# Kernel optimization log

Measured on AMD Instinct MI355X. Metric: run time of the kernel, lower is better.

The kernel has to match this reference:

```python
import jax, jax.numpy as jnp
import numpy as np
from jax import lax

B, IN, HID, OUT = 32, 1024, 1024, 1024
NN, NS, NH = 1000, 64, 4          # n_paths/num_neurons, num_states, attn heads
NSTEPS = NS * 10                   # 640 SDE steps
GROUPS = 10                        # python loop groups in original BICEPLayer
T_HORIZON = 1.0


def setup_inputs() -> dict:
    key = jax.random.key(0)
    ks = jax.random.split(key, 16)
    def n(k, shape, s=0.02):
        return jax.random.normal(k, shape, jnp.float32) * s
    z = lambda *s: jnp.zeros(s, jnp.float32)
    return {
        "x": jax.random.normal(ks[0], (B, IN), jnp.float32),
        "noise": jax.random.normal(ks[1], (B, NN, NSTEPS), jnp.float32),
        "W_emb": n(ks[2], (NN * NS, IN)), "b_emb": z(NN * NS),
        "w_ih": n(ks[3], (4 * NS, NS), 0.1), "w_hh": n(ks[4], (4 * NS, NS), 0.1),
        "b_ih": z(4 * NS), "b_hh": z(4 * NS),
        "w_in": n(ks[5], (3 * NS, NS), 0.1), "b_in": z(3 * NS),
        "w_out": n(ks[6], (NS, NS), 0.1), "b_out": z(NS),
        "W_fix": jax.random.normal(ks[7], (HID, NS), jnp.float32),  # torch.randn dim-fix linear
        "W_inproj": n(ks[8], (NN, IN)), "b_inproj": z(NN),
        "conv_w": n(ks[9], (1, NSTEPS + 1, 3), 0.05), "conv_b": z(1),
        "W_bout": n(ks[10], (HID, NN)), "b_bout": z(HID),
        "decay_rate": jnp.float32(0.1),
        "W_fuse": n(ks[11], (HID, 2 * HID)), "b_fuse": z(HID),
        "W_proj": n(ks[12], (OUT, HID)), "b_proj": z(OUT),
    }


def _forward(x, noise, W_emb, b_emb, w_ih, w_hh, b_ih, b_hh, w_in, b_in,
             w_out, b_out, W_fix, W_inproj, b_inproj, conv_w, conv_b,
             W_bout, b_bout, decay_rate, W_fuse, b_fuse, W_proj, b_proj):
    Bsz = x.shape[0]
    # ---- ENN branch ----
    ns = (x @ W_emb.T + b_emb).reshape(Bsz, NN, NS)

    def lstm_step(carry, xt):  # xt [B, NS]
        h, c = carry
        g = xt @ w_ih.T + b_ih + h @ w_hh.T + b_hh
        i, f, gg, o = jnp.split(g, 4, axis=-1)  # torch gate order i,f,g,o
        c = jax.nn.sigmoid(f) * c + jax.nn.sigmoid(i) * jnp.tanh(gg)
        h = jax.nn.sigmoid(o) * jnp.tanh(c)
        return (h, c), h

    h0 = jnp.zeros((Bsz, NS), x.dtype)
    _, hs = lax.scan(lstm_step, (h0, h0), jnp.swapaxes(ns, 0, 1))
    lstm_out = jnp.swapaxes(hs, 0, 1)  # [B, NN, NS]

    qkv = lstm_out @ w_in.T + b_in
    q, k, v = jnp.split(qkv, 3, axis=-1)
    dh = NS // NH
    heads = lambda t: t.reshape(Bsz, NN, NH, dh).transpose(0, 2, 1, 3)
    q, k, v = heads(q), heads(k), heads(v)
    scores = jnp.einsum('bhqd,bhkd->bhqk', q, k) * (1.0 / float(np.sqrt(dh)))
    attn = jax.nn.softmax(scores, axis=-1)
    ctx = jnp.einsum('bhqk,bhkd->bhqd', attn, v).transpose(0, 2, 1, 3).reshape(Bsz, NN, NS)
    attended = ctx @ w_out.T + b_out
    attn_w = attn.mean(axis=1)  # torch MHA averages heads by default

    enn = jax.nn.relu(attended.mean(axis=1))  # [B, NS]
    enn = enn @ W_fix.T                        # [B, HID] (random dim-fix linear, no bias)

    # ---- BICEP branch (vectorized Brownian SDE over all batches/paths) ----
    fb = jax.nn.sigmoid(x @ W_inproj.T + b_inproj)  # [B, NN]
    # original uses .item() -> detached scalars, only first 10 feedback values
    f_full = jnp.repeat(lax.stop_gradient(fb[:, :GROUPS]), NN // GROUPS, axis=1)  # [B, NN]
    dt = T_HORIZON / NSTEPS
    sq = float(np.sqrt(dt))
    dr = lax.stop_gradient(decay_rate)  # .item() in original

    def sde_step(Xc, nt):  # Euler-Maruyama: dX = -decay*X dt + feedback dW
        Xn = Xc * (1.0 - dr * dt) + f_full * sq * nt
        return Xn, Xn

    _, Xs = lax.scan(sde_step, jnp.zeros((Bsz, NN), x.dtype), jnp.moveaxis(noise, 2, 0))
    paths = jnp.concatenate([jnp.zeros((1, Bsz, NN), x.dtype), Xs], axis=0)  # [T+1, B, NN]
    paths = jnp.moveaxis(paths, 0, 1)  # [B, NSTEPS+1, NN] -> channels = time

    agg = lax.conv_general_dilated(paths, conv_w, (1,), ((1, 1),),
                                   dimension_numbers=('NCH', 'OIH', 'NCH'))
    agg = agg[:, 0, :] + conv_b  # [B, NN]
    bicep = agg @ W_bout.T + b_bout  # [B, HID]

    # ---- fusion (dropout is identity in eval) ----
    fused = jnp.concatenate([enn, bicep], axis=-1) @ W_fuse.T + b_fuse
    output = fused @ W_proj.T + b_proj
    return output, enn, bicep, attn_w


def reference(x, noise, W_emb, b_emb, w_ih, w_hh, b_ih, b_hh, w_in, b_in,
              w_out, b_out, W_fix, W_inproj, b_inproj, conv_w, conv_b,
              W_bout, b_bout, decay_rate, W_fuse, b_fuse, W_proj, b_proj):
    return _forward(x, noise, W_emb, b_emb, w_ih, w_hh, b_ih, b_hh, w_in, b_in,
                    w_out, b_out, W_fix, W_inproj, b_inproj, conv_w, conv_b,
                    W_bout, b_bout, decay_rate, W_fuse, b_fuse, W_proj, b_proj)
```

## Files before the change

kernel.cpp:

```cpp
#include <hip/hip_runtime.h>
#include <hip/hip_bf16.h>
#include <math.h>

#define BATCH 32

typedef short bf16x8 __attribute__((ext_vector_type(8)));
typedef float f32x4 __attribute__((ext_vector_type(4)));

__device__ __forceinline__ float sigmoidf_(float x){ return 1.0f/(1.0f + __expf(-x)); }
__device__ __forceinline__ unsigned short f2bf(float x){
  unsigned u = __float_as_uint(x);
  unsigned r = (u + 0x7FFFu + ((u>>16)&1u)) >> 16;
  return (unsigned short)r;
}
__device__ __forceinline__ float sig2(float x){
  return __builtin_amdgcn_rcpf(1.0f + __builtin_amdgcn_exp2f(x * -1.44269504f));
}
__device__ __forceinline__ float tanh2(float x){
  return 1.0f - 2.0f*__builtin_amdgcn_rcpf(1.0f + __builtin_amdgcn_exp2f(x * 2.88539008f));
}
__device__ __forceinline__ f32x4 unpk4(uint2 p){
  f32x4 r;
  r[0] = __uint_as_float(p.x << 16);
  r[1] = __uint_as_float(p.x & 0xffff0000u);
  r[2] = __uint_as_float(p.y << 16);
  r[3] = __uint_as_float(p.y & 0xffff0000u);
  return r;
}

__global__ __launch_bounds__(256) void k12_emb_pre(const float* __restrict__ x,
    const float* __restrict__ W_emb, const float* __restrict__ b_emb,
    const float* __restrict__ W_inp, const float* __restrict__ b_inp,
    const float* __restrict__ w_ih, const float* __restrict__ b_ih, const float* __restrict__ b_hh,
    float* __restrict__ fb, unsigned short* __restrict__ preh)
{
  __shared__ __align__(16) float xl[BATCH][256];
  __shared__ float red[64][33];
  __shared__ __align__(16) float nsl2[32][68];
  const int tid = threadIdx.x;
  const int jt = tid >> 4;
  const int seg = tid & 15;
  const int blk = blockIdx.x;
  const bool isemb = (blk < 1000);
  const float* wr_[4];
  #pragma unroll
  for (int jj=0;jj<4;jj++){
    if (isemb) wr_[jj] = W_emb + (size_t)(blk*64 + jt*4 + jj) * 1024;
    else { int t2 = (blk-1000)*64 + jt*4 + jj; if (t2 > 999) t2 = 999; wr_[jj] = W_inp + (size_t)t2 * 1024; }
  }
  float acc[4][32];
  #pragma unroll
  for (int jj=0;jj<4;jj++)
    #pragma unroll
    for (int b=0;b<32;b++) acc[jj][b]=0.f;
  for (int c=0;c<4;c++){
    __syncthreads();
    for (int f = tid; f < 2048; f += 256){
      int b = f >> 6; int col = (f & 63) << 2;
      *(float4*)&xl[b][col] = *(const float4*)&x[b*1024 + c*256 + col];
    }
    __syncthreads();
    #pragma unroll
    for (int ii=0; ii<4; ii++){
      float4 wv[4];
      #pragma unroll
      for (int jj=0;jj<4;jj++) wv[jj] = *(const float4*)&wr_[jj][c*256 + ii*64 + seg*4];
      #pragma unroll
      for (int b=0;b<32;b++){
        float4 xv = *(const float4*)&xl[b][ii*64 + seg*4];
        #pragma unroll
        for (int jj=0;jj<4;jj++){
          acc[jj][b] = fmaf(wv[jj].x, xv.x, acc[jj][b]);
          acc[jj][b] = fmaf(wv[jj].y, xv.y, acc[jj][b]);
          acc[jj][b] = fmaf(wv[jj].z, xv.z, acc[jj][b]);
          acc[jj][b] = fmaf(wv[jj].w, xv.w, acc[jj][b]);
        }
      }
    }
  }
  #pragma unroll
  for (int jj=0;jj<4;jj++){
    #pragma unroll
    for (int b=0;b<32;b++){
      float v = acc[jj][b];
      v += __shfl_xor(v, 1);
      v += __shfl_xor(v, 2);
      v += __shfl_xor(v, 4);
      v += __shfl_xor(v, 8);
      if (seg == 0) red[jt*4+jj][b] = v;
    }
  }
  __syncthreads();
  #pragma unroll
  for (int it=0; it<8; it++){
    int idx = it*256 + tid;
    int b = idx >> 6, jl = idx & 63;
    float v = red[jl][b];
    if (isemb){
      nsl2[b][jl] = v + b_emb[blk*64 + jl];
    } else {
      int jin = (blk-1000)*64 + jl;
      if (jin < 1000) fb[b*1000 + jin] = sigmoidf_(v + b_inp[jin]);
    }
  }
  if (!isemb) return;
  __syncthreads();
  const int j = tid;
  const int pcol = (j & 63)*4 + (j >> 6);
  float wreg[64];
  const float* wr = w_ih + j*64;
  #pragma unroll
  for (int k=0;k<64;k+=4){
    float4 v = *(const float4*)&wr[k];
    wreg[k]=v.x; wreg[k+1]=v.y; wreg[k+2]=v.z; wreg[k+3]=v.w;
  }
  float bias = b_ih[j] + b_hh[j];
  for (int b=0;b<32;b++){
    float a0=0,a1=0,a2=0,a3=0;
    #pragma unroll
    for (int k=0;k<64;k+=4){
      float4 nv = *(const float4*)&nsl2[b][k];
      a0=fmaf(nv.x,wreg[k],a0);   a1=fmaf(nv.y,wreg[k+1],a1);
      a2=fmaf(nv.z,wreg[k+2],a2); a3=fmaf(nv.w,wreg[k+3],a3);
    }
    preh[(size_t)(b*1000+blk)*256 + pcol] = f2bf((a0+a1)+(a2+a3) + bias);
  }
}

__global__ __launch_bounds__(256) void k3_lstm_sde(
  const unsigned short* __restrict__ preh, unsigned short* __restrict__ lstmT,
  const float* __restrict__ w_hh,
  const float* __restrict__ noise, const float* __restrict__ fb,
  const float* __restrict__ conv_w, const float* __restrict__ decay_p,
  float* __restrict__ S0, float* __restrict__ S1, float* __restrict__ S2)
{
  __shared__ __align__(16) unsigned char shraw[8192];
  const int tid = threadIdx.x;
  if (blockIdx.x < 8){
    unsigned short* hls = (unsigned short*)shraw;
    const int b0 = blockIdx.x * 4;
    const int w = tid >> 6;
    const int lane = tid & 63;
    const int nl = lane & 15;
    const int g  = lane >> 4;
    const int r  = nl & 3;
    for (int i = tid; i < 640; i += 256) hls[i] = 0;
    bf16x8 A[4][2];
    #pragma unroll
    for (int tt=0; tt<4; tt++){
      const int rt = 4*w + tt;
      const float* wsrc = w_hh + (size_t)((nl&3)*64 + 4*rt + (nl>>2))*64;
      #pragma unroll
      for (int kh=0; kh<2; kh++){
        bf16x8 f;
        #pragma unroll
        for (int i=0;i<8;i++) f[i] = (short)f2bf(wsrc[kh*32 + 8*g + i]);
        A[tt][kh] = f;
      }
    }
    const int jg = 16*w + 4*(nl>>2) + g;
    const int bat = b0 + r;
    const unsigned short* pp = preh + (size_t)bat*256000 + jg*4;
    uint2 P[4];
    #pragma unroll
    for (int s=0;s<4;s++) P[s] = *(const uint2*)(pp + (size_t)s*256);
    const int rdA = r*80 + (g ^ r)*8;
    const int wr = r*80 + ((jg>>3) ^ r)*8 + (jg & 7);
    unsigned short* lt = lstmT + ((size_t)bat*64 + jg)*1000;
    const bool s1 = (nl & 4) != 0, s2 = (nl & 8) != 0;
    float c = 0.f;
    unsigned ph[4];
    __syncthreads();
    int buf = 0;
    for (int tb=0; tb<1000; tb+=8){
      #pragma unroll
      for (int u=0;u<8;u++){
        bf16x8 B0 = *(const bf16x8*)&hls[buf*320 + rdA];
        bf16x8 B1 = *(const bf16x8*)&hls[buf*320 + rdA + 32];
        const int slot = u & 3;
        f32x4 Cp = unpk4(P[slot]);
        int tp = tb + u + 4; if (tp > 999) tp = 999;
        P[slot] = *(const uint2*)(pp + (size_t)tp*256);
        f32x4 D0 = __builtin_amdgcn_mfma_f32_16x16x32_bf16(A[0][0], B0, Cp, 0,0,0);
        D0 = __builtin_amdgcn_mfma_f32_16x16x32_bf16(A[0][1], B1, D0, 0,0,0);
        f32x4 D1 = __builtin_amdgcn_mfma_f32_16x16x32_bf16(A[1][0], B0, Cp, 0,0,0);
        D1 = __builtin_amdgcn_mfma_f32_16x16x32_bf16(A[1][1], B1, D1, 0,0,0);
        f32x4 D2 = __builtin_amdgcn_mfma_f32_16x16x32_bf16(A[2][0], B0, Cp, 0,0,0);
        D2 = __builtin_amdgcn_mfma_f32_16x16x32_bf16(A[2][1], B1, D2, 0,0,0);
        f32x4 D3 = __builtin_amdgcn_mfma_f32_16x16x32_bf16(A[3][0], B0, Cp, 0,0,0);
        D3 = __builtin_amdgcn_mfma_f32_16x16x32_bf16(A[3][1], B1, D3, 0,0,0);
        float g0 = s2 ? (s1 ? D3[0] : D2[0]) : (s1 ? D1[0] : D0[0]);
        float g1 = s2 ? (s1 ? D3[1] : D2[1]) : (s1 ? D1[1] : D0[1]);
        float g2 = s2 ? (s1 ? D3[2] : D2[2]) : (s1 ? D1[2] : D0[2]);
        float g3 = s2 ? (s1 ? D3[3] : D2[3]) : (s1 ? D1[3] : D0[3]);
        float iv = sig2(g0), fv = sig2(g1), gv = tanh2(g2), ov = sig2(g3);
        c = fv*c + iv*gv;
        float h = ov * tanh2(c);
        unsigned hb = f2bf(h);
        if (u & 1) ph[u>>1] |= hb << 16; else ph[u>>1] = hb;
        hls[(buf^1)*320 + wr] = (unsigned short)hb;
        asm volatile("s_waitcnt lgkmcnt(0)" ::: "memory");
        __builtin_amdgcn_s_barrier();
        asm volatile("" ::: "memory");
        buf ^= 1;
      }
      *(uint4*)(lt + tb) = make_uint4(ph[0], ph[1], ph[2], ph[3]);
    }
  } else {
    float* cw = (float*)shraw;
    for (int f = tid; f < 641*3; f += 256) cw[f] = conv_w[f];
    __syncthreads();
    int idx = (blockIdx.x - 8)*256 + tid;
    if (idx < 32000){
      int b = idx / 1000, n = idx - b*1000;
      float fcoef = fb[b*1000 + (n/100)];
      float dr = decay_p[0];
      const float dt = 1.0f/640.0f;
      float adec = 1.0f - dr*dt;
      float g = fcoef * sqrtf(dt);
      const float* nptr = noise + (size_t)idx * 640;
      float X=0.f, s0=0.f, s1=0.f, s2=0.f;
      for (int t0=0;t0<640;t0+=4){
        float4 nz = *(const float4*)&nptr[t0];
        float nv[4] = {nz.x, nz.y, nz.z, nz.w};
        #pragma unroll
        for (int u=0;u<4;u++){
          X = fmaf(adec, X, g*nv[u]);
          int t = t0 + u + 1;
          s0 = fmaf(cw[t*3+0], X, s0);
          s1 = fmaf(cw[t*3+1], X, s1);
          s2 = fmaf(cw[t*3+2], X, s2);
        }
      }
      S0[idx]=s0; S1[idx]=s1; S2[idx]=s2;
    }
  }
}

__global__ __launch_bounds__(256) void k4_qkv(const unsigned short* __restrict__ lstmT,
  const float* __restrict__ w_in, const float* __restrict__ b_in,
  unsigned short* __restrict__ Qb, unsigned short* __restrict__ Kb, unsigned short* __restrict__ Vt)
{
  __shared__ __align__(16) float wl[192*64];
  __shared__ float bl[192];
  const int tid = threadIdx.x;
  for (int i=tid;i<3072;i+=256) ((float4*)wl)[i] = ((const float4*)w_in)[i];
  if (tid < 192) bl[tid] = b_in[tid];
  __syncthreads();
  const int rl = tid & 127, dh = tid >> 7;
  const int rn = blockIdx.x*128 + rl;
  const int b = rn >> 10, n = rn & 1023;
  const bool valid = (n < 1000);
  const int nc = valid ? n : 999;
  float row[64];
  #pragma unroll
  for (int k=0;k<64;k++){
    unsigned v = lstmT[((size_t)b*64 + k)*1000 + nc];
    row[k] = valid ? __uint_as_float(v << 16) : 0.f;
  }
  for (int dc=0; dc<12; dc++){
    const int d0 = dh*96 + dc*8;
    float acc[8];
    #pragma unroll
    for (int u=0;u<8;u++) acc[u] = bl[d0+u];
    #pragma unroll
    for (int k=0;k<64;k+=4){
      float4 rv = *(const float4*)&row[k];
      #pragma unroll
      for (int u=0;u<8;u++){
        float4 wv = *(const float4*)&wl[(d0+u)*64 + k];
        acc[u]=fmaf(rv.x,wv.x,acc[u]); acc[u]=fmaf(rv.y,wv.y,acc[u]);
        acc[u]=fmaf(rv.z,wv.z,acc[u]); acc[u]=fmaf(rv.w,wv.w,acc[u]);
      }
    }
    unsigned short pk[8];
    #pragma unroll
    for (int u=0;u<8;u++) pk[u] = valid ? f2bf(acc[u]) : (unsigned short)0;
    if (d0 + 8 <= 64){
      *(bf16x8*)&Qb[(size_t)rn*64 + d0] = *(bf16x8*)pk;
    } else if (d0 + 8 <= 128){
      *(bf16x8*)&Kb[(size_t)rn*64 + (d0-64)] = *(bf16x8*)pk;
    } else {
      int dv = d0 - 128;
      #pragma unroll
      for (int u=0;u<8;u++) Vt[((size_t)b*64 + dv+u)*1024 + n] = pk[u];
    }
  }
}

__global__ __launch_bounds__(256) void k5_attn(
  const unsigned short* __restrict__ Qb, const unsigned short* __restrict__ Kb,
  const unsigned short* __restrict__ Vt,
  float* __restrict__ attn_w, float* __restrict__ ctx)
{
  const int b = blockIdx.x;
  const int qblk = blockIdx.y;
  const int wid = threadIdx.x >> 6;
  const int lane = threadIdx.x & 63;
  const int r = lane & 15, gq = lane >> 4;
  const int q = qblk*64 + wid*16 + r;
  const bool gok = (gq < 2);
  const float SC2 = 0.25f * 1.44269504f;
  const f32x4 z4 = {0.f,0.f,0.f,0.f};

  bf16x8 qf[4];
  #pragma unroll
  for (int h=0; h<4; h++){
    bf16x8 f = {};
    if (gok) f = *(const bf16x8*)&Qb[(((size_t)b*1024)+q)*64 + h*16 + 8*gq];
    qf[h] = f;
  }
  float snv[4];
  #pragma unroll
  for (int h=0; h<4; h++){
    float es = 0.f;
    for (int kk=0; kk<63; kk++){
      bf16x8 kf = {};
      if (gok) kf = *(const bf16x8*)&Kb[(((size_t)b*1024)+(kk*16+r))*64 + h*16 + 8*gq];
      f32x4 d = __builtin_amdgcn_mfma_f32_16x16x32_bf16(kf, qf[h], z4, 0,0,0);
      float e0=__builtin_amdgcn_exp2f(d[0]*SC2), e1=__builtin_amdgcn_exp2f(d[1]*SC2);
      float e2=__builtin_amdgcn_exp2f(d[2]*SC2), e3=__builtin_amdgcn_exp2f(d[3]*SC2);
      if (kk == 62 && !gok){ e0=0;e1=0;e2=0;e3=0; }
      es += (e0+e1)+(e2+e3);
    }
    es += __shfl_xor(es, 16);
    es += __shfl_xor(es, 32);
    snv[h] = 0.25f / es;
  }
  f32x4 cacc[4] = {};
  float* awrow = attn_w + (size_t)b*1000000;
  for (int kkp=0; kkp<31; kkp++){
    const int kk = kkp*2;
    f32x4 aacc0 = z4, aacc1 = z4;
    #pragma unroll
    for (int h=0; h<4; h++){
      bf16x8 kf0 = {}, kf1 = {};
      if (gok){
        kf0 = *(const bf16x8*)&Kb[(((size_t)b*1024)+(kk*16+r))*64 + h*16 + 8*gq];
        kf1 = *(const bf16x8*)&Kb[(((size_t)b*1024)+(kk*16+16+r))*64 + h*16 + 8*gq];
      }
      f32x4 d0 = __builtin_amdgcn_mfma_f32_16x16x32_bf16(kf0, qf[h], z4, 0,0,0);
      f32x4 d1 = __builtin_amdgcn_mfma_f32_16x16x32_bf16(kf1, qf[h], z4, 0,0,0);
      float p00=__builtin_amdgcn_exp2f(d0[0]*SC2)*snv[h], p01=__builtin_amdgcn_exp2f(d0[1]*SC2)*snv[h];
      float p02=__builtin_amdgcn_exp2f(d0[2]*SC2)*snv[h], p03=__builtin_amdgcn_exp2f(d0[3]*SC2)*snv[h];
      float p10=__builtin_amdgcn_exp2f(d1[0]*SC2)*snv[h], p11=__builtin_amdgcn_exp2f(d1[1]*SC2)*snv[h];
      float p12=__builtin_amdgcn_exp2f(d1[2]*SC2)*snv[h], p13=__builtin_amdgcn_exp2f(d1[3]*SC2)*snv[h];
      aacc0[0]+=p00; aacc0[1]+=p01; aacc0[2]+=p02; aacc0[3]+=p03;
      aacc1[0]+=p10; aacc1[1]+=p11; aacc1[2]+=p12; aacc1[3]+=p13;
      const int slo = (r + 32*gq) & 63;
      const int shi = (slo + 16) & 63;
      {
        unsigned pa = (unsigned)f2bf(p00) | ((unsigned)f2bf(p01) << 16);
        unsigned pb = (unsigned)f2bf(p02) | ((unsigned)f2bf(p03) << 16);
        int b0_ = __shfl((int)pa, slo), b1_ = __shfl((int)pb, slo);
        int b2_ = __shfl((int)pa, shi), b3_ = __shfl((int)pb, shi);
        union { int i[4]; bf16x8 v; } pu;
        pu.i[0]=b0_; pu.i[1]=b1_; pu.i[2]=b2_; pu.i[3]=b3_;
        bf16x8 pfrag = pu.v;
        if (!gok) pfrag = (bf16x8){};
        bf16x8 vf = {};
        if (gok) vf = *(const bf16x8*)&Vt[(((size_t)b*64) + h*16 + r)*1024 + kk*16 + 8*gq];
        cacc[h] = __builtin_amdgcn_mfma_f32_16x16x32_bf16(vf, pfrag, cacc[h], 0,0,0);
      }
      {
        unsigned pa = (unsigned)f2bf(p10) | ((unsigned)f2bf(p11) << 16);
        unsigned pb = (unsigned)f2bf(p12) | ((unsigned)f2bf(p13) << 16);
        int b0_ = __shfl((int)pa, slo), b1_ = __shfl((int)pb, slo);
        int b2_ = __shfl((int)pa, shi), b3_ = __shfl((int)pb, shi);
        union { int i[4]; bf16x8 v; } pu;
        pu.i[0]=b0_; pu.i[1]=b1_; pu.i[2]=b2_; pu.i[3]=b3_;
        bf16x8 pfrag = pu.v;
        if (!gok) pfrag = (bf16x8){};
        bf16x8 vf = {};
        if (gok) vf = *(const bf16x8*)&Vt[(((size_t)b*64) + h*16 + r)*1024 + kk*16 + 16 + 8*gq];
        cacc[h] = __builtin_amdgcn_mfma_f32_16x16x32_bf16(vf, pfrag, cacc[h], 0,0,0);
      }
    }
    if (q < 1000){
      *(f32x4*)&awrow[(size_t)q*1000 + kk*16 + 4*gq] = aacc0;
      *(f32x4*)&awrow[(size_t)q*1000 + kk*16 + 16 + 4*gq] = aacc1;
    }
  }
  {
    const int kk = 62;
    f32x4 aacc = z4;
    #pragma unroll
    for (int h=0; h<4; h++){
      bf16x8 kf = {};
      if (gok) kf = *(const bf16x8*)&Kb[(((size_t)b*1024)+(kk*16+r))*64 + h*16 + 8*gq];
      f32x4 d = __builtin_amdgcn_mfma_f32_16x16x32_bf16(kf, qf[h], z4, 0,0,0);
      float p0=__builtin_amdgcn_exp2f(d[0]*SC2)*snv[h], p1=__builtin_amdgcn_exp2f(d[1]*SC2)*snv[h];
      float p2=__builtin_amdgcn_exp2f(d[2]*SC2)*snv[h], p3=__builtin_amdgcn_exp2f(d[3]*SC2)*snv[h];
      if (!gok){ p0=0;p1=0;p2=0;p3=0; }
      aacc[0]+=p0; aacc[1]+=p1; aacc[2]+=p2; aacc[3]+=p3;
      unsigned pa = (unsigned)f2bf(p0) | ((unsigned)f2bf(p1) << 16);
      unsigned pb = (unsigned)f2bf(p2) | ((unsigned)f2bf(p3) << 16);
      int slo = (r + 32*gq) & 63;
      int shi = (slo + 16) & 63;
      int b0_ = __shfl((int)pa, slo), b1_ = __shfl((int)pb, slo);
      int b2_ = __shfl((int)pa, shi), b3_ = __shfl((int)pb, shi);
      union { int i[4]; bf16x8 v; } pu;
      pu.i[0]=b0_; pu.i[1]=b1_; pu.i[2]=b2_; pu.i[3]=b3_;
      bf16x8 pfrag = pu.v;
      if (!gok) pfrag = (bf16x8){};
      bf16x8 vf = {};
      if (gok) vf = *(const bf16x8*)&Vt[(((size_t)b*64) + h*16 + r)*1024 + kk*16 + 8*gq];
      cacc[h] = __builtin_amdgcn_mfma_f32_16x16x32_bf16(vf, pfrag, cacc[h], 0,0,0);
    }
    if (q < 1000 && gok){
      *(f32x4*)&awrow[(size_t)q*1000 + kk*16 + 4*gq] = aacc;
    }
  }
  if (q < 1000){
    #pragma unroll
    for (int h=0; h<4; h++){
      f32x4 cv = cacc[h];
      cv[0]*=4.f; cv[1]*=4.f; cv[2]*=4.f; cv[3]*=4.f;
      *(f32x4*)&ctx[(((size_t)b*1024)+q)*64 + h*16 + 4*gq] = cv;
    }
  }
}

__global__ __launch_bounds__(256) void k67_psum_agg(const float* __restrict__ ctx,
  float* __restrict__ psum,
  const float* __restrict__ S0, const float* __restrict__ S1,
  const float* __restrict__ S2, const float* __restrict__ conv_b, float* __restrict__ agg)
{
  if (blockIdx.x < 256){
    __shared__ float part[256];
    const int blk = blockIdx.x;
    const int b = blk >> 3, seg = blk & 7;
    const int t = threadIdx.x, d = t & 63, sg = t >> 6;
    float s = 0.f;
    const int nend = seg*125 + 125;
    for (int n = seg*125 + sg; n < nend; n += 4)
      s += ctx[(((size_t)b*1024)+n)*64 + d];
    part[t] = s;
    __syncthreads();
    if (t < 64) psum[((size_t)b*8 + seg)*64 + t] = part[t] + part[64+t] + part[128+t] + part[192+t];
  } else {
    int i = (blockIdx.x - 256)*256 + threadIdx.x;
    if (i >= 32000) return;
    int n = i % 1000;
    float v = S1[i] + conv_b[0];
    if (n > 0)   v += S0[i-1];
    if (n < 999) v += S2[i+1];
    agg[i] = v;
  }
}

__global__ __launch_bounds__(256) void k68_enn_bicep(const float* __restrict__ psum,
  const float* __restrict__ w_out, const float* __restrict__ b_out,
  const float* __restrict__ W_fix, float* __restrict__ enn_out,
  const float* __restrict__ agg, const float* __restrict__ W_bout,
  const float* __restrict__ b_bout, float* __restrict__ bicep)
{
  if (blockIdx.x < 32){
    __shared__ __align__(16) float csum[64];
    __shared__ __align__(16) float epre[64];
    int b = blockIdx.x, t = threadIdx.x;
    if (t < 64){
      float a = 0;
      #pragma unroll
      for (int s2=0;s2<8;s2++) a += psum[((size_t)b*8 + s2)*64 + t];
      csum[t] = a;
    }
    __syncthreads();
    if (t < 64){
      const float* wr = w_out + t*64;
      float a = 0;
      #pragma unroll
      for (int k=0;k<64;k++) a = fmaf(csum[k], wr[k], a);
      epre[t] = fmaxf(a*(1.0f/1000.0f) + b_out[t], 0.0f);
    }
    __syncthreads();
    for (int m = t; m < 1024; m += 256){
      const float* fr = W_fix + m*64;
      float a = 0;
      #pragma unroll
      for (int k=0;k<64;k+=4){
        float4 e4 = *(const float4*)&epre[k];
        float4 f4 = *(const float4*)&fr[k];
        a=fmaf(e4.x,f4.x,a); a=fmaf(e4.y,f4.y,a); a=fmaf(e4.z,f4.z,a); a=fmaf(e4.w,f4.w,a);
      }
      enn_out[b*1024 + m] = a;
    }
  } else {
    int gt = (blockIdx.x - 32)*256 + threadIdx.x;
    int bb = gt & 31, m = gt >> 5;
    const float* wr = W_bout + (size_t)m*1000;
    const float* ar = agg + bb*1000;
    float a = 0;
    for (int n=0;n<1000;n+=4){
      float4 w4 = *(const float4*)&wr[n];
      float4 a4 = *(const float4*)&ar[n];
      a=fmaf(w4.x,a4.x,a); a=fmaf(w4.y,a4.y,a); a=fmaf(w4.z,a4.z,a); a=fmaf(w4.w,a4.w,a);
    }
    bicep[bb*1024 + m] = a + b_bout[m];
  }
}

__global__ __launch_bounds__(256) void k9_fuse(const float* __restrict__ enn, const float* __restrict__ bic,
  const float* __restrict__ W_fuse, const float* __restrict__ b_fuse, float* __restrict__ fused)
{
  int gt = blockIdx.x*256 + threadIdx.x;
  int bb = gt & 31, m = gt >> 5;
  const float* er = enn + bb*1024;
  const float* br = bic + bb*1024;
  const float* wr = W_fuse + (size_t)m*2048;
  float a = 0;
  for (int jj=0;jj<1024;jj+=4){
    float4 e4 = *(const float4*)&er[jj];
    float4 w4 = *(const float4*)&wr[jj];
    a=fmaf(e4.x,w4.x,a); a=fmaf(e4.y,w4.y,a); a=fmaf(e4.z,w4.z,a); a=fmaf(e4.w,w4.w,a);
  }
  for (int jj=0;jj<1024;jj+=4){
    float4 b4 = *(const float4*)&br[jj];
    float4 w4 = *(const float4*)&wr[1024+jj];
    a=fmaf(b4.x,w4.x,a); a=fmaf(b4.y,w4.y,a); a=fmaf(b4.z,w4.z,a); a=fmaf(b4.w,w4.w,a);
  }
  fused[bb*1024 + m] = a + b_fuse[m];
}

__global__ __launch_bounds__(256) void k10_proj(const float* __restrict__ fused,
  const float* __restrict__ W_proj, const float* __restrict__ b_proj, float* __restrict__ outp)
{
  int gt = blockIdx.x*256 + threadIdx.x;
  int bb = gt & 31, m = gt >> 5;
  const float* fr = fused + bb*1024;
  const float* wr = W_proj + (size_t)m*1024;
  float a = 0;
  for (int jj=0;jj<1024;jj+=4){
    float4 f4 = *(const float4*)&fr[jj];
    float4 w4 = *(const float4*)&wr[jj];
    a=fmaf(f4.x,w4.x,a); a=fmaf(f4.y,w4.y,a); a=fmaf(f4.z,w4.z,a); a=fmaf(f4.w,w4.w,a);
  }
  outp[bb*1024 + m] = a + b_proj[m];
}

extern "C" void kernel_launch(void* const* d_in, const int* in_sizes, int n_in,
                              void* d_out, int out_size, void* d_ws, size_t ws_size,
                              hipStream_t stream)
{
  const float* x       = (const float*)d_in[0];
  const float* noise   = (const float*)d_in[1];
  const float* W_emb   = (const float*)d_in[2];
  const float* b_emb   = (const float*)d_in[3];
  const float* w_ih    = (const float*)d_in[4];
  const float* w_hh    = (const float*)d_in[5];
  const float* b_ih    = (const float*)d_in[6];
  const float* b_hh    = (const float*)d_in[7];
  const float* w_in    = (const float*)d_in[8];
  const float* b_in    = (const float*)d_in[9];
  const float* w_out   = (const float*)d_in[10];
  const float* b_out   = (const float*)d_in[11];
  const float* W_fix   = (const float*)d_in[12];
  const float* W_inp   = (const float*)d_in[13];
  const float* b_inp   = (const float*)d_in[14];
  const float* conv_w  = (const float*)d_in[15];
  const float* conv_b  = (const float*)d_in[16];
  const float* W_bout  = (const float*)d_in[17];
  const float* b_bout  = (const float*)d_in[18];
  const float* decay   = (const float*)d_in[19];
  const float* W_fuse  = (const float*)d_in[20];
  const float* b_fuse  = (const float*)d_in[21];
  const float* W_proj  = (const float*)d_in[22];
  const float* b_proj  = (const float*)d_in[23];

  float* out       = (float*)d_out;
  float* enn_out   = out + 32768;
  float* bicep_out = out + 65536;
  float* attn_out  = out + 98304;

  float* ws    = (float*)d_ws;
  float* fb    = ws;
  unsigned short* preh  = (unsigned short*)(ws + 2080000);
  float* psum  = ws + 6200000;
  unsigned short* lstmT = (unsigned short*)(ws + 10272000);
  float* ctx   = ws + 12320000;
  float* S0    = ws + 14417152;
  float* S1    = ws + 14449152;
  float* S2    = ws + 14481152;
  float* agg   = ws + 14513152;
  float* fused = ws + 14545152;
  unsigned short* Qb = (unsigned short*)(ws + 14577920);
  unsigned short* Kb = Qb + 2097152;
  unsigned short* Vt = Kb + 2097152;

  k12_emb_pre<<<1016, 256, 0, stream>>>(x, W_emb, b_emb, W_inp, b_inp,
                                        w_ih, b_ih, b_hh, fb, preh);
  k3_lstm_sde<<<133, 256, 0, stream>>>(preh, lstmT, w_hh, noise, fb, conv_w, decay, S0, S1, S2);
  k4_qkv<<<256, 256, 0, stream>>>(lstmT, w_in, b_in, Qb, Kb, Vt);
  k5_attn<<<dim3(32,16), 256, 0, stream>>>(Qb, Kb, Vt, attn_out, ctx);
  k67_psum_agg<<<382, 256, 0, stream>>>(ctx, psum, S0, S1, S2, conv_b, agg);
  k68_enn_bicep<<<160, 256, 0, stream>>>(psum, w_out, b_out, W_fix, enn_out,
                                         agg, W_bout, b_bout, bicep_out);
  k9_fuse<<<128, 256, 0, stream>>>(enn_out, bicep_out, W_fuse, b_fuse, fused);
  k10_proj<<<128, 256, 0, stream>>>(fused, W_proj, b_proj, out);
}
```

Before: 985.9 us.

## Use bf16 MFMA for embedding GEMM and split w_ih projection into separate kernel

The fused embedding plus input-projection kernel is split in two. The first kernel computes the large x@W_emb and x@W_inproj GEMMs with bf16 MFMA 16x16x32 instructions, converting fp32 weights and inputs to bf16 on the fly, instead of scalar fp32 FMAs with LDS staging. The second kernel computes the LSTM input-gate pre-activations from the stored ns buffer. This is meant to remove the FMA-bound inner loop, at the cost of an extra launch, a round trip of ns through global memory, and reduced GEMM precision.

```diff
diff --git a/kernel.cpp b/kernel.cpp
--- a/kernel.cpp
+++ b/kernel.cpp
@@ -27,85 +27,82 @@
   r[3] = __uint_as_float(p.y & 0xffff0000u);
   return r;
 }
-
-__global__ __launch_bounds__(256) void k12_emb_pre(const float* __restrict__ x,
+__device__ __forceinline__ bf16x8 pack8(float4 a, float4 b){
+  bf16x8 f;
+  f[0]=(short)f2bf(a.x); f[1]=(short)f2bf(a.y); f[2]=(short)f2bf(a.z); f[3]=(short)f2bf(a.w);
+  f[4]=(short)f2bf(b.x); f[5]=(short)f2bf(b.y); f[6]=(short)f2bf(b.z); f[7]=(short)f2bf(b.w);
+  return f;
+}
+
+__global__ __launch_bounds__(256) void k1_emb(const float* __restrict__ x,
     const float* __restrict__ W_emb, const float* __restrict__ b_emb,
     const float* __restrict__ W_inp, const float* __restrict__ b_inp,
-    const float* __restrict__ w_ih, const float* __restrict__ b_ih, const float* __restrict__ b_hh,
-    float* __restrict__ fb, unsigned short* __restrict__ preh)
-{
-  __shared__ __align__(16) float xl[BATCH][256];
-  __shared__ float red[64][33];
-  __shared__ __align__(16) float nsl2[32][68];
+    float* __restrict__ ns, float* __restrict__ fb)
+{
   const int tid = threadIdx.x;
-  const int jt = tid >> 4;
-  const int seg = tid & 15;
+  const int w = tid >> 6, lane = tid & 63;
+  const int nl = lane & 15, g = lane >> 4;
   const int blk = blockIdx.x;
   const bool isemb = (blk < 1000);
-  const float* wr_[4];
+  const int j0 = (isemb ? blk : (blk - 1000))*64 + w*16;
+  const int arow = j0 + nl;
+  const float* wrow;
+  if (isemb) wrow = W_emb + (size_t)arow*1024;
+  else       wrow = W_inp + (size_t)(arow > 999 ? 999 : arow)*1024;
+  f32x4 D0, D1;
   #pragma unroll
-  for (int jj=0;jj<4;jj++){
-    if (isemb) wr_[jj] = W_emb + (size_t)(blk*64 + jt*4 + jj) * 1024;
-    else { int t2 = (blk-1000)*64 + jt*4 + jj; if (t2 > 999) t2 = 999; wr_[jj] = W_inp + (size_t)t2 * 1024; }
-  }
-  float acc[4][32];
-  #pragma unroll
-  for (int jj=0;jj<4;jj++)
-    #pragma unroll
-    for (int b=0;b<32;b++) acc[jj][b]=0.f;
-  for (int c=0;c<4;c++){
-    __syncthreads();
-    for (int f = tid; f < 2048; f += 256){
-      int b = f >> 6; int col = (f & 63) << 2;
-      *(float4*)&xl[b][col] = *(const float4*)&x[b*1024 + c*256 + col];
-    }
-    __syncthreads();
-    #pragma unroll
-    for (int ii=0; ii<4; ii++){
-      float4 wv[4];
-      #pragma unroll
-      for (int jj=0;jj<4;jj++) wv[jj] = *(const float4*)&wr_[jj][c*256 + ii*64 + seg*4];
-      #pragma unroll
-      for (int b=0;b<32;b++){
-        float4 xv = *(const float4*)&xl[b][ii*64 + seg*4];
-        #pragma unroll
-        for (int jj=0;jj<4;jj++){
-          acc[jj][b] = fmaf(wv[jj].x, xv.x, acc[jj][b]);
-          acc[jj][b] = fmaf(wv[jj].y, xv.y, acc[jj][b]);
-          acc[jj][b] = fmaf(wv[jj].z, xv.z, acc[jj][b]);
-          acc[jj][b] = fmaf(wv[jj].w, xv.w, acc[jj][b]);
-        }
-      }
-    }
-  }
-  #pragma unroll
-  for (int jj=0;jj<4;jj++){
-    #pragma unroll
-    for (int b=0;b<32;b++){
-      float v = acc[jj][b];
-      v += __shfl_xor(v, 1);
-      v += __shfl_xor(v, 2);
-      v += __shfl_xor(v, 4);
-      v += __shfl_xor(v, 8);
-      if (seg == 0) red[jt*4+jj][b] = v;
-    }
-  }
-  __syncthreads();
-  #pragma unroll
-  for (int it=0; it<8; it++){
-    int idx = it*256 + tid;
-    int b = idx >> 6, jl = idx & 63;
-    float v = red[jl][b];
-    if (isemb){
-      nsl2[b][jl] = v + b_emb[blk*64 + jl];
-    } else {
-      int jin = (blk-1000)*64 + jl;
-      if (jin < 1000) fb[b*1000 + jin] = sigmoidf_(v + b_inp[jin]);
-    }
-  }
-  if (!isemb) return;
-  __syncthreads();
+  for (int q=0;q<4;q++){
+    int jr = j0 + 4*g + q;
+    float bb = isemb ? b_emb[jr] : b_inp[jr > 999 ? 999 : jr];
+    D0[q] = bb; D1[q] = bb;
+  }
+  const float* xr0 = x + nl*1024;
+  const float* xr1 = x + (nl+16)*1024;
+  for (int kc=0; kc<8; kc++){
+    float4 wa[4][2];
+    #pragma unroll
+    for (int s=0;s<4;s++){
+      const float* p = wrow + kc*128 + s*32 + 8*g;
+      wa[s][0] = *(const float4*)p;
+      wa[s][1] = *(const float4*)(p+4);
+    }
+    #pragma unroll
+    for (int s=0;s<4;s++){
+      const int k0 = kc*128 + s*32 + 8*g;
+      float4 x00 = *(const float4*)(xr0 + k0);
+      float4 x01 = *(const float4*)(xr0 + k0 + 4);
+      float4 x10 = *(const float4*)(xr1 + k0);
+      float4 x11 = *(const float4*)(xr1 + k0 + 4);
+      bf16x8 A  = pack8(wa[s][0], wa[s][1]);
+      bf16x8 B0 = pack8(x00, x01);
+      bf16x8 B1 = pack8(x10, x11);
+      D0 = __builtin_amdgcn_mfma_f32_16x16x32_bf16(A, B0, D0, 0,0,0);
+      D1 = __builtin_amdgcn_mfma_f32_16x16x32_bf16(A, B1, D1, 0,0,0);
+    }
+  }
+  if (isemb){
+    *(f32x4*)&ns[(size_t)nl*64000 + j0 + 4*g] = D0;
+    *(f32x4*)&ns[(size_t)(nl+16)*64000 + j0 + 4*g] = D1;
+  } else {
+    #pragma unroll
+    for (int q=0;q<4;q++){
+      int jr = j0 + 4*g + q;
+      if (jr < 1000){
+        fb[nl*1000 + jr]      = sig2(D0[q]);
+        fb[(nl+16)*1000 + jr] = sig2(D1[q]);
+      }
+    }
+  }
+}
+
+__global__ __launch_bounds__(256) void k2_pre(const float* __restrict__ ns,
+   const float* __restrict__ w_ih, const float* __restrict__ b_ih, const float* __restrict__ b_hh,
+   unsigned short* __restrict__ preh)
+{
+  __shared__ __align__(16) float nsl[64*64];
+  const int tid = threadIdx.x;
   const int j = tid;
+  const int rn0 = blockIdx.x * 64;
   const int pcol = (j & 63)*4 + (j >> 6);
   float wreg[64];
   const float* wr = w_ih + j*64;
@@ -115,15 +112,18 @@
     wreg[k]=v.x; wreg[k+1]=v.y; wreg[k+2]=v.z; wreg[k+3]=v.w;
   }
   float bias = b_ih[j] + b_hh[j];
-  for (int b=0;b<32;b++){
+  const float4* src = (const float4*)(ns + (size_t)rn0*64);
+  for (int i=tid; i<64*16; i+=256) ((float4*)nsl)[i] = src[i];
+  __syncthreads();
+  for (int r=0;r<64;r++){
     float a0=0,a1=0,a2=0,a3=0;
     #pragma unroll
     for (int k=0;k<64;k+=4){
-      float4 nv = *(const float4*)&nsl2[b][k];
+      float4 nv = *(const float4*)&nsl[r*64+k];
       a0=fmaf(nv.x,wreg[k],a0);   a1=fmaf(nv.y,wreg[k+1],a1);
       a2=fmaf(nv.z,wreg[k+2],a2); a3=fmaf(nv.w,wreg[k+3],a3);
     }
-    preh[(size_t)(b*1000+blk)*256 + pcol] = f2bf((a0+a1)+(a2+a3) + bias);
+    preh[(size_t)(rn0+r)*256 + pcol] = f2bf((a0+a1)+(a2+a3) + bias);
   }
 }
 
@@ -574,6 +574,7 @@
 
   float* ws    = (float*)d_ws;
   float* fb    = ws;
+  float* ns    = ws + 32000;
   unsigned short* preh  = (unsigned short*)(ws + 2080000);
   float* psum  = ws + 6200000;
   unsigned short* lstmT = (unsigned short*)(ws + 10272000);
@@ -587,8 +588,8 @@
   unsigned short* Kb = Qb + 2097152;
   unsigned short* Vt = Kb + 2097152;
 
-  k12_emb_pre<<<1016, 256, 0, stream>>>(x, W_emb, b_emb, W_inp, b_inp,
-                                        w_ih, b_ih, b_hh, fb, preh);
+  k1_emb<<<1016, 256, 0, stream>>>(x, W_emb, b_emb, W_inp, b_inp, ns, fb);
+  k2_pre<<<500, 256, 0, stream>>>(ns, w_ih, b_ih, b_hh, preh);
   k3_lstm_sde<<<133, 256, 0, stream>>>(preh, lstmT, w_hh, noise, fb, conv_w, decay, S0, S1, S2);
   k4_qkv<<<256, 256, 0, stream>>>(lstmT, w_in, b_in, Qb, Kb, Vt);
   k5_attn<<<dim3(32,16), 256, 0, stream>>>(Qb, Kb, Vt, attn_out, ctx);
```

Result: faster. 816.0 us (-17.2%).
